# Performance work log

Hardware: AMD Instinct MI355X
Metric: run time of the kernel (lower is better)

The kernel has to match this reference:

```python
import jax, jax.numpy as jnp
import numpy as np

B, S, HID = 1, 4096, 2304
NH, NKV, HD = 8, 4, 256
SW = 2048                 # sliding window (layer_idx=0 -> active)
SOFTCAP = 50.0
SCALE = 256.0 ** -0.5     # query_pre_attn_scalar ** -0.5
THETA = 10000.0
NEG = -1e30


def rotate_half(x):
    x1, x2 = jnp.split(x, 2, axis=-1)
    return jnp.concatenate([-x2, x1], axis=-1)


def setup_inputs() -> dict:
    key = jax.random.key(0)
    ks = jax.random.split(key, 5)
    hidden_states = jax.random.normal(ks[0], (B, S, HID), jnp.float32)
    position_ids = jnp.tile(jnp.arange(S, dtype=jnp.int32)[None, :], (B, 1))
    Wq = 0.02 * jax.random.normal(ks[1], (NH * HD, HID), jnp.float32)
    Wk = 0.02 * jax.random.normal(ks[2], (NKV * HD, HID), jnp.float32)
    Wv = 0.02 * jax.random.normal(ks[3], (NKV * HD, HID), jnp.float32)
    Wo = 0.02 * jax.random.normal(ks[4], (HID, NH * HD), jnp.float32)
    return {"hidden_states": hidden_states, "position_ids": position_ids,
            "Wq": Wq, "Wk": Wk, "Wv": Wv, "Wo": Wo}


def reference(hidden_states, position_ids, Wq, Wk, Wv, Wo):
    b, s, _ = hidden_states.shape
    # fused QKV projections (torch Linear: y = x @ W.T)
    q = jnp.einsum('bsh,oh->bso', hidden_states, Wq).reshape(b, s, NH, HD).transpose(0, 2, 1, 3)
    k = jnp.einsum('bsh,oh->bso', hidden_states, Wk).reshape(b, s, NKV, HD).transpose(0, 2, 1, 3)
    v = jnp.einsum('bsh,oh->bso', hidden_states, Wv).reshape(b, s, NKV, HD).transpose(0, 2, 1, 3)

    # rotary embedding
    inv_freq = 1.0 / (THETA ** (jnp.arange(0, HD, 2, dtype=jnp.float32) / HD))
    freqs = position_ids.astype(jnp.float32)[:, :, None] * inv_freq[None, None, :]  # [b,s,hd/2]
    emb = jnp.concatenate([freqs, freqs], axis=-1)                                  # [b,s,hd]
    cos = jnp.cos(emb)[:, None, :, :]  # [b,1,s,hd]
    sin = jnp.sin(emb)[:, None, :, :]
    q = q * cos + rotate_half(q) * sin
    k = k * cos + rotate_half(k) * sin

    # GQA: repeat kv heads
    groups = NH // NKV
    k = jnp.repeat(k, groups, axis=1)  # [b,nh,s,hd]
    v = jnp.repeat(v, groups, axis=1)

    scores = jnp.einsum('bhqd,bhkd->bhqk', q, k) * SCALE
    scores = SOFTCAP * jnp.tanh(scores / SOFTCAP)  # logit softcapping

    i = jnp.arange(s)[:, None]
    j = jnp.arange(s)[None, :]
    mask = (j <= i) & ((i - j) < SW)               # causal + sliding window
    scores = jnp.where(mask[None, None], scores, NEG)

    attn = jax.nn.softmax(scores, axis=-1)
    out = jnp.einsum('bhqk,bhkd->bhqd', attn, v)
    out = out.transpose(0, 2, 1, 3).reshape(b, s, NH * HD)
    return jnp.einsum('bso,ho->bsh', out, Wo)
```

## Files before the change

### kernel.cpp

```cpp
#include <hip/hip_runtime.h>
#include <hip/hip_bf16.h>

typedef __attribute__((ext_vector_type(8))) short short8;
typedef __attribute__((ext_vector_type(4))) short short4v;
typedef __attribute__((ext_vector_type(4))) float floatx4;

#define S_LEN 4096
#define HIDDEN 2304
#define NHEADS 8
#define NKVH 4
#define HDIM 256
#define SWIN 2048

static __device__ __forceinline__ short bf16bits(float x) {
    __hip_bfloat16 h = __float2bfloat16(x);
    return __builtin_bit_cast(short, h);
}
static __device__ __forceinline__ float bits2f(short b) {
    return __bfloat162float(__builtin_bit_cast(__hip_bfloat16, b));
}

static __device__ __forceinline__ void gload_lds16(const short* g, short* l) {
    __builtin_amdgcn_global_load_lds((const __attribute__((address_space(1))) void*)g,
                                     (__attribute__((address_space(3))) void*)l,
                                     16, 0, 0);
}

__global__ __launch_bounds__(256) void cast_f32_bf16(const float* __restrict__ in,
                                                     short* __restrict__ out, int n4) {
    int i = blockIdx.x * 256 + threadIdx.x;
    if (i >= n4) return;
    float4 v = ((const float4*)in)[i];
    short4v o;
    o.x = bf16bits(v.x); o.y = bf16bits(v.y); o.z = bf16bits(v.z); o.w = bf16bits(v.w);
    ((short4v*)out)[i] = o;
}

__global__ __launch_bounds__(256) void cast_wqkv(const float* __restrict__ Wq,
                                                 const float* __restrict__ Wk,
                                                 const float* __restrict__ Wv,
                                                 short* __restrict__ dst) {
    const int NQ4 = 1179648, NK4 = 589824;
    int i = blockIdx.x * 256 + threadIdx.x;
    const float4* src;
    if (i < NQ4)            src = (const float4*)Wq + i;
    else if (i < NQ4 + NK4) src = (const float4*)Wk + (i - NQ4);
    else                    src = (const float4*)Wv + (i - NQ4 - NK4);
    float4 v = *src;
    short4v o;
    o.x = bf16bits(v.x); o.y = bf16bits(v.y); o.z = bf16bits(v.z); o.w = bf16bits(v.w);
    ((short4v*)dst)[i] = o;
}

template<int MODE>
__global__ __launch_bounds__(256) void gemm_lds(const short* __restrict__ A,
                                                const short* __restrict__ B,
                                                void* __restrict__ Cp,
                                                int M, int N, int K, int ldc)
{
    __shared__ __align__(16) short lA[128 * 32];
    __shared__ __align__(16) short lB[128 * 32];
    int tid  = threadIdx.x;
    int lane = tid & 63;
    int wave = tid >> 6;
    int col  = lane & 15;
    int quad = lane >> 4;
    int m_base = blockIdx.y * 128;
    int n_base = blockIdx.x * 128;
    int wm = (wave >> 1) * 64;
    int wn = (wave & 1) * 64;

    int srow = wave * 32 + (lane >> 2);
    int scol = (lane & 3) * 8;
    const short* gA0 = A + (size_t)(m_base + srow) * K + scol;
    const short* gA1 = gA0 + (size_t)16 * K;
    const short* gB0 = B + (size_t)(n_base + srow) * K + scol;
    const short* gB1 = gB0 + (size_t)16 * K;
    short* lA0 = lA + wave * 1024;
    short* lB0 = lB + wave * 1024;

    floatx4 acc[4][4] = {};

    for (int k0 = 0; k0 < K; k0 += 32) {
        __syncthreads();
        gload_lds16(gA0 + k0, lA0);
        gload_lds16(gA1 + k0, lA0 + 512);
        gload_lds16(gB0 + k0, lB0);
        gload_lds16(gB1 + k0, lB0 + 512);
        __syncthreads();

        short8 af[4], bf[4];
        #pragma unroll
        for (int t = 0; t < 4; ++t) {
            af[t] = *(const short8*)(lA + (wm + t*16 + col) * 32 + quad * 8);
            bf[t] = *(const short8*)(lB + (wn + t*16 + col) * 32 + quad * 8);
        }
        #pragma unroll
        for (int mt = 0; mt < 4; ++mt)
            #pragma unroll
            for (int nt = 0; nt < 4; ++nt)
                acc[mt][nt] = __builtin_amdgcn_mfma_f32_16x16x32_bf16(af[mt], bf[nt], acc[mt][nt], 0, 0, 0);
    }

    #pragma unroll
    for (int mt = 0; mt < 4; ++mt) {
        #pragma unroll
        for (int nt = 0; nt < 4; ++nt) {
            int n  = n_base + wn + nt*16 + col;
            int m0 = m_base + wm + mt*16 + quad*4;
            if (MODE == 0) {
                short* C = (short*)Cp;
                #pragma unroll
                for (int r = 0; r < 4; ++r)
                    C[(size_t)(m0 + r) * ldc + n] = bf16bits(acc[mt][nt][r]);
            } else {
                float* C = (float*)Cp;
                #pragma unroll
                for (int r = 0; r < 4; ++r)
                    C[(size_t)(m0 + r) * ldc + n] = acc[mt][nt][r];
            }
        }
    }
}

__global__ __launch_bounds__(256) void gemm_qkv(const short* __restrict__ A,
                                                const short* __restrict__ B,
                                                short* __restrict__ QKV,
                                                short* __restrict__ Vt)
{
    __shared__ __align__(16) short lA[128 * 32];
    __shared__ __align__(16) short lB[128 * 32];
    const int K = HIDDEN;
    int tid  = threadIdx.x;
    int lane = tid & 63;
    int wave = tid >> 6;
    int col  = lane & 15;
    int quad = lane >> 4;
    int m_base = blockIdx.y * 128;
    int n_base = blockIdx.x * 128;
    int wm = (wave >> 1) * 64;
    int wn = (wave & 1) * 64;

    int srow = wave * 32 + (lane >> 2);
    int scol = (lane & 3) * 8;
    const short* gA0 = A + (size_t)(m_base + srow) * K + scol;
    const short* gA1 = gA0 + (size_t)16 * K;
    const short* gB0 = B + (size_t)(n_base + srow) * K + scol;
    const short* gB1 = gB0 + (size_t)16 * K;
    short* lA0 = lA + wave * 1024;
    short* lB0 = lB + wave * 1024;

    floatx4 acc[4][4] = {};

    for (int k0 = 0; k0 < K; k0 += 32) {
        __syncthreads();
        gload_lds16(gA0 + k0, lA0);
        gload_lds16(gA1 + k0, lA0 + 512);
        gload_lds16(gB0 + k0, lB0);
        gload_lds16(gB1 + k0, lB0 + 512);
        __syncthreads();

        short8 af[4], bf[4];
        #pragma unroll
        for (int t = 0; t < 4; ++t) {
            af[t] = *(const short8*)(lA + (wm + t*16 + col) * 32 + quad * 8);
            bf[t] = *(const short8*)(lB + (wn + t*16 + col) * 32 + quad * 8);
        }
        #pragma unroll
        for (int mt = 0; mt < 4; ++mt)
            #pragma unroll
            for (int nt = 0; nt < 4; ++nt)
                acc[mt][nt] = __builtin_amdgcn_mfma_f32_16x16x32_bf16(af[mt], bf[nt], acc[mt][nt], 0, 0, 0);
    }

    #pragma unroll
    for (int mt = 0; mt < 4; ++mt) {
        #pragma unroll
        for (int nt = 0; nt < 4; ++nt) {
            int n  = n_base + wn + nt*16 + col;
            int m0 = m_base + wm + mt*16 + quad*4;
            if (n_base + wn + nt*16 < 3072) {
                #pragma unroll
                for (int r = 0; r < 4; ++r)
                    QKV[(size_t)(m0 + r) * 4096 + n] = bf16bits(acc[mt][nt][r]);
            } else {
                short4v v;
                v.x = bf16bits(acc[mt][nt][0]);
                v.y = bf16bits(acc[mt][nt][1]);
                v.z = bf16bits(acc[mt][nt][2]);
                v.w = bf16bits(acc[mt][nt][3]);
                *(short4v*)(Vt + (size_t)(n - 3072) * 4096 + m0) = v;
            }
        }
    }
}

__global__ __launch_bounds__(256) void rope_kernel(short* __restrict__ QKV,
                                                   const int* __restrict__ pos)
{
    int t = blockIdx.x * 256 + threadIdx.x;
    int d   = t & 127;
    int rem = t >> 7;
    int hh  = rem % 12;
    int s   = rem / 12;
    float p   = (float)pos[s];
    float inv = __expf(-9.210340371976184f * ((float)d * (1.0f/128.0f)));
    float ang = p * inv;
    float sn, cs;
    sincosf(ang, &sn, &cs);
    short* row = QKV + (size_t)s * 4096 + hh * 256;
    float x1 = bits2f(row[d]);
    float x2 = bits2f(row[d + 128]);
    row[d]       = bf16bits(x1 * cs - x2 * sn);
    row[d + 128] = bf16bits(x2 * cs + x1 * sn);
}

__global__ __launch_bounds__(128) void attn_kernel(const short* __restrict__ QKV,
                                                   const short* __restrict__ Vt,
                                                   short* __restrict__ Ob)
{
    __shared__ __align__(16) short lK[64 * 256];
    __shared__ __align__(16) short lV[256 * 64];
    __shared__ __align__(16) short lP[2][32 * 64];
    int tid  = threadIdx.x;
    int lane = tid & 63;
    int wave = tid >> 6;
    int col  = lane & 15;
    int quad = lane >> 4;
    int bid  = blockIdx.x;
    int g     = bid >> 7;
    int chunk = (bid >> 1) & 63;
    int h     = g * 2 + (bid & 1);
    int qb = chunk * 64;
    int q0 = qb + wave * 32;

    short8 qf[2][8];
    #pragma unroll
    for (int mt = 0; mt < 2; ++mt) {
        const short* Qrow = QKV + (size_t)(q0 + mt*16 + col) * 4096 + h * 256;
        #pragma unroll
        for (int c = 0; c < 8; ++c)
            qf[mt][c] = *(const short8*)(Qrow + c*32 + quad*8);
    }

    int keyL = wave * 32 + (lane >> 5);
    int segK = lane & 31;
    const short* pK[4];
    #pragma unroll
    for (int j = 0; j < 4; ++j) {
        int key = keyL + 2 * j;
        pK[j] = QKV + (size_t)key * 4096 + 2048 + g * 256 + ((segK ^ (key & 7)) << 3);
    }
    short* dK = lK + wave * 32 * 256;

    int dL   = wave * 128 + (lane >> 3);
    int segV = lane & 7;
    const short* pV = Vt + (size_t)(g * 256 + dL) * 4096 + ((segV ^ (dL & 7)) << 3);
    short* dV = lV + wave * 128 * 64;

    floatx4 o[2][16] = {};
    float psum[2][4] = {};

    int kb_start = qb - (SWIN - 1);
    if (kb_start < 0) kb_start = 0;
    kb_start &= ~63;

    for (int kb = kb_start; kb < qb + 64; kb += 64) {
        __syncthreads();
        #pragma unroll
        for (int i = 0; i < 16; ++i)
            gload_lds16(pK[i & 3] + (size_t)(kb + 8 * (i >> 2)) * 4096, dK + 2*i*256);
        #pragma unroll
        for (int i = 0; i < 16; ++i)
            gload_lds16(pV + (size_t)(8 * i) * 4096 + kb, dV + 8*i*64);
        __syncthreads();

        floatx4 sc[2][4] = {};
        #pragma unroll
        for (int c = 0; c < 8; ++c) {
            short8 kf[4];
            #pragma unroll
            for (int kt = 0; kt < 4; ++kt)
                kf[kt] = *(const short8*)(lK + (kt*16 + col) * 256
                                             + ((c*32 + quad*8) ^ ((col & 7) << 3)));
            #pragma unroll
            for (int mt = 0; mt < 2; ++mt)
                #pragma unroll
                for (int kt = 0; kt < 4; ++kt)
                    sc[mt][kt] = __builtin_amdgcn_mfma_f32_16x16x32_bf16(qf[mt][c], kf[kt], sc[mt][kt], 0, 0, 0);
        }

        bool full = (kb + 64 <= q0) && (kb + SWIN >= q0 + 32);
#define SOFTMAX_BODY(MASKED)                                                        \
        _Pragma("unroll")                                                           \
        for (int mt = 0; mt < 2; ++mt)                                              \
            _Pragma("unroll")                                                       \
            for (int kt = 0; kt < 4; ++kt)                                          \
                _Pragma("unroll")                                                   \
                for (int r = 0; r < 4; ++r) {                                       \
                    float y  = sc[mt][kt][r] * 0.0625f;                             \
                    float x2 = y * y * 4.0e-4f;                                     \
                    float sv = y * (1.0f + x2 * (-0.33333333f + x2 * 0.13333333f)); \
                    float p  = __expf(sv - 12.0f);                                  \
                    if (MASKED) {                                                   \
                        int i = q0 + mt*16 + quad*4 + r;                            \
                        int j = kb + kt*16 + col;                                   \
                        bool v = (j <= i) && ((i - j) < SWIN);                      \
                        p = v ? p : 0.0f;                                           \
                    }                                                               \
                    psum[mt][r] += p;                                               \
                    int q = mt*16 + quad*4 + r;                                     \
                    lP[wave][q*64 + ((kt*16 + col) ^ ((q & 7) << 3))] = bf16bits(p);\
                }
        if (full) { SOFTMAX_BODY(false) } else { SOFTMAX_BODY(true) }
#undef SOFTMAX_BODY

        __threadfence_block();

        short8 pa[2][2];
        #pragma unroll
        for (int mt = 0; mt < 2; ++mt)
            #pragma unroll
            for (int kh = 0; kh < 2; ++kh)
                pa[mt][kh] = *(const short8*)(&lP[wave][(mt*16 + col) * 64
                                                 + ((kh*32 + quad*8) ^ ((col & 7) << 3))]);

        #pragma unroll
        for (int nt = 0; nt < 16; ++nt) {
            short8 vf0 = *(const short8*)(lV + (nt*16 + col) * 64
                                             + ((quad*8)      ^ ((col & 7) << 3)));
            short8 vf1 = *(const short8*)(lV + (nt*16 + col) * 64
                                             + ((32 + quad*8) ^ ((col & 7) << 3)));
            #pragma unroll
            for (int mt = 0; mt < 2; ++mt) {
                o[mt][nt] = __builtin_amdgcn_mfma_f32_16x16x32_bf16(pa[mt][0], vf0, o[mt][nt], 0, 0, 0);
                o[mt][nt] = __builtin_amdgcn_mfma_f32_16x16x32_bf16(pa[mt][1], vf1, o[mt][nt], 0, 0, 0);
            }
        }
    }

    #pragma unroll
    for (int off = 1; off < 16; off <<= 1)
        #pragma unroll
        for (int mt = 0; mt < 2; ++mt)
            #pragma unroll
            for (int r = 0; r < 4; ++r)
                psum[mt][r] += __shfl_xor(psum[mt][r], off, 64);

    #pragma unroll
    for (int mt = 0; mt < 2; ++mt)
        #pragma unroll
        for (int nt = 0; nt < 16; ++nt)
            #pragma unroll
            for (int r = 0; r < 4; ++r) {
                int i = q0 + mt*16 + quad*4 + r;
                Ob[(size_t)i * 2048 + h*256 + nt*16 + col] = bf16bits(o[mt][nt][r] / psum[mt][r]);
            }
}

extern "C" void kernel_launch(void* const* d_in, const int* in_sizes, int n_in,
                              void* d_out, int out_size, void* d_ws, size_t ws_size,
                              hipStream_t stream)
{
    const float* X  = (const float*)d_in[0];
    const int*  pos = (const int*)d_in[1];
    const float* Wq = (const float*)d_in[2];
    const float* Wk = (const float*)d_in[3];
    const float* Wv = (const float*)d_in[4];
    const float* Wo = (const float*)d_in[5];
    float* out = (float*)d_out;
    char* ws = (char*)d_ws;

    short* Xb    = (short*)(ws + 0);
    short* Wqkvb = (short*)(ws + 18874368);
    short* Wob   = (short*)(ws + 37748736);
    short* QKVb  = (short*)(ws + 47185920);
    short* Vt    = (short*)(ws + 80740352);
    short* Ob    = (short*)(ws + 0);

    cast_f32_bf16<<<9216, 256, 0, stream>>>(X,  Xb,  2359296);
    cast_wqkv<<<9216, 256, 0, stream>>>(Wq, Wk, Wv, Wqkvb);
    cast_f32_bf16<<<4608, 256, 0, stream>>>(Wo, Wob, 1179648);

    gemm_qkv<<<dim3(32,32), 256, 0, stream>>>(Xb, Wqkvb, QKVb, Vt);

    rope_kernel<<<24576, 256, 0, stream>>>(QKVb, pos);

    attn_kernel<<<512, 128, 0, stream>>>(QKVb, Vt, Ob);

    gemm_lds<2><<<dim3(18,32), 256, 0, stream>>>(Ob, Wob, out, 4096, 2304, 2048, 2304);
}
```

Before: 486.4 us.

## Split attention key range across blocks and share K/V tiles between GQA heads

Each attention block now runs four waves covering both query heads of a KV group, so each K/V tile loaded into LDS is reused by two heads. Blocks are paired so each handles half of the key tiles in the sliding window. They write unnormalized fp16 partial outputs and per-row softmax sums to the workspace. A new combine kernel adds the two partials and divides by the summed denominators to produce the bf16 attention output. This evens out work across blocks and improves K/V reuse, at the cost of an extra partial-output round trip through memory and fp16 range risk on unnormalized accumulators.

```diff
diff --git a/kernel.cpp b/kernel.cpp
--- a/kernel.cpp
+++ b/kernel.cpp
@@ -4,6 +4,7 @@
 typedef __attribute__((ext_vector_type(8))) short short8;
 typedef __attribute__((ext_vector_type(4))) short short4v;
 typedef __attribute__((ext_vector_type(4))) float floatx4;
+typedef __attribute__((ext_vector_type(8))) _Float16 half8;
 
 #define S_LEN 4096
 #define HIDDEN 2304
@@ -215,13 +216,14 @@
     row[d + 128] = bf16bits(x2 * cs + x1 * sn);
 }
 
-__global__ __launch_bounds__(128) void attn_kernel(const short* __restrict__ QKV,
+__global__ __launch_bounds__(256) void attn_kernel(const short* __restrict__ QKV,
                                                    const short* __restrict__ Vt,
-                                                   short* __restrict__ Ob)
+                                                   _Float16* __restrict__ Opart,
+                                                   float* __restrict__ Psp)
 {
     __shared__ __align__(16) short lK[64 * 256];
     __shared__ __align__(16) short lV[256 * 64];
-    __shared__ __align__(16) short lP[2][32 * 64];
+    __shared__ __align__(16) short lP[4][32 * 64];
     int tid  = threadIdx.x;
     int lane = tid & 63;
     int wave = tid >> 6;
@@ -230,9 +232,10 @@
     int bid  = blockIdx.x;
     int g     = bid >> 7;
     int chunk = (bid >> 1) & 63;
-    int h     = g * 2 + (bid & 1);
+    int half  = bid & 1;
+    int h     = g * 2 + (wave >> 1);
     int qb = chunk * 64;
-    int q0 = qb + wave * 32;
+    int q0 = qb + (wave & 1) * 32;
 
     short8 qf[2][8];
     #pragma unroll
@@ -243,7 +246,7 @@
             qf[mt][c] = *(const short8*)(Qrow + c*32 + quad*8);
     }
 
-    int keyL = wave * 32 + (lane >> 5);
+    int keyL = wave * 16 + (lane >> 5);
     int segK = lane & 31;
     const short* pK[4];
     #pragma unroll
@@ -251,27 +254,31 @@
         int key = keyL + 2 * j;
         pK[j] = QKV + (size_t)key * 4096 + 2048 + g * 256 + ((segK ^ (key & 7)) << 3);
     }
-    short* dK = lK + wave * 32 * 256;
-
-    int dL   = wave * 128 + (lane >> 3);
+    short* dK = lK + wave * 16 * 256;
+
+    int dL   = wave * 64 + (lane >> 3);
     int segV = lane & 7;
     const short* pV = Vt + (size_t)(g * 256 + dL) * 4096 + ((segV ^ (dL & 7)) << 3);
-    short* dV = lV + wave * 128 * 64;
+    short* dV = lV + wave * 64 * 64;
 
     floatx4 o[2][16] = {};
     float psum[2][4] = {};
 
-    int kb_start = qb - (SWIN - 1);
-    if (kb_start < 0) kb_start = 0;
-    kb_start &= ~63;
-
-    for (int kb = kb_start; kb < qb + 64; kb += 64) {
-        __syncthreads();
-        #pragma unroll
-        for (int i = 0; i < 16; ++i)
+    int kb_lo = qb - (SWIN - 1);
+    if (kb_lo < 0) kb_lo = 0;
+    kb_lo &= ~63;
+    int T  = ((qb + 64) - kb_lo) >> 6;
+    int T0 = T >> 1;
+    int kb_beg = kb_lo + (half ? T0 * 64 : 0);
+    int kb_end = kb_lo + (half ? T * 64 : T0 * 64);
+
+    for (int kb = kb_beg; kb < kb_end; kb += 64) {
+        __syncthreads();
+        #pragma unroll
+        for (int i = 0; i < 8; ++i)
             gload_lds16(pK[i & 3] + (size_t)(kb + 8 * (i >> 2)) * 4096, dK + 2*i*256);
         #pragma unroll
-        for (int i = 0; i < 16; ++i)
+        for (int i = 0; i < 8; ++i)
             gload_lds16(pV + (size_t)(8 * i) * 4096 + kb, dV + 8*i*64);
         __syncthreads();
 
@@ -347,6 +354,7 @@
             for (int r = 0; r < 4; ++r)
                 psum[mt][r] += __shfl_xor(psum[mt][r], off, 64);
 
+    _Float16* Op = Opart + (size_t)half * (4096 * 2048);
     #pragma unroll
     for (int mt = 0; mt < 2; ++mt)
         #pragma unroll
@@ -354,8 +362,34 @@
             #pragma unroll
             for (int r = 0; r < 4; ++r) {
                 int i = q0 + mt*16 + quad*4 + r;
-                Ob[(size_t)i * 2048 + h*256 + nt*16 + col] = bf16bits(o[mt][nt][r] / psum[mt][r]);
+                Op[(size_t)i * 2048 + h*256 + nt*16 + col] = (_Float16)o[mt][nt][r];
             }
+    if (col == 0) {
+        #pragma unroll
+        for (int mt = 0; mt < 2; ++mt)
+            #pragma unroll
+            for (int r = 0; r < 4; ++r)
+                Psp[half * 32768 + h * 4096 + q0 + mt*16 + quad*4 + r] = psum[mt][r];
+    }
+}
+
+__global__ __launch_bounds__(256) void combine_kernel(const _Float16* __restrict__ O0,
+                                                      const _Float16* __restrict__ O1,
+                                                      const float* __restrict__ Ps,
+                                                      short* __restrict__ Ob)
+{
+    int t = blockIdx.x * 256 + threadIdx.x;
+    size_t base = (size_t)t * 8;
+    int q = (int)(base >> 11);
+    int h = (int)((base >> 8) & 7);
+    float inv = 1.0f / (Ps[h * 4096 + q] + Ps[32768 + h * 4096 + q]);
+    half8 a = *(const half8*)(O0 + base);
+    half8 b = *(const half8*)(O1 + base);
+    short8 o;
+    #pragma unroll
+    for (int j = 0; j < 8; ++j)
+        o[j] = bf16bits(((float)a[j] + (float)b[j]) * inv);
+    *(short8*)(Ob + base) = o;
 }
 
 extern "C" void kernel_launch(void* const* d_in, const int* in_sizes, int n_in,
@@ -376,7 +410,9 @@
     short* Wob   = (short*)(ws + 37748736);
     short* QKVb  = (short*)(ws + 47185920);
     short* Vt    = (short*)(ws + 80740352);
-    short* Ob    = (short*)(ws + 0);
+    _Float16* Opart = (_Float16*)(ws + 0);
+    float*    Psp   = (float*)(ws + 33554432);
+    short*    Ob    = (short*)(ws + 0);
 
     cast_f32_bf16<<<9216, 256, 0, stream>>>(X,  Xb,  2359296);
     cast_wqkv<<<9216, 256, 0, stream>>>(Wq, Wk, Wv, Wqkvb);
@@ -386,7 +422,9 @@
 
     rope_kernel<<<24576, 256, 0, stream>>>(QKVb, pos);
 
-    attn_kernel<<<512, 128, 0, stream>>>(QKVb, Vt, Ob);
+    attn_kernel<<<512, 256, 0, stream>>>(QKVb, Vt, Opart, Psp);
+
+    combine_kernel<<<4096, 256, 0, stream>>>(Opart, Opart + (size_t)4096*2048, Psp, Ob);
 
     gemm_lds<2><<<dim3(18,32), 256, 0, stream>>>(Ob, Wob, out, 4096, 2304, 2048, 2304);
 }
```

New measurement: 473.5 us. 1.03x faster.
